# Optimization experiments

Hardware: AMD Instinct MI355X
Metric: run time of the kernel (lower is better)

## Reference

```python
import jax, jax.numpy as jnp
import numpy as np

EMA_BETA = 0.9
NUM_HEADS = 16

def causal_prefix_ema(x, beta):
    # x: [b, t, d]; s_t = beta*s_{t-1} + (1-beta)*x_t, s_{-1}=0
    def step(s, xt):
        s = beta * s + (1.0 - beta) * xt
        return s, s
    s0 = jnp.zeros_like(x[:, 0, :])
    _, ys = jax.lax.scan(step, s0, jnp.swapaxes(x, 0, 1))  # [t, b, d]
    return jnp.swapaxes(ys, 0, 1)

def setup_inputs() -> dict:
    key = jax.random.key(0)
    ks = jax.random.split(key, 9)
    b, t, d = 2, 1024, 2048
    sc = lambda fan_in: 1.0 / np.sqrt(fan_in)
    return {
        "x": jax.random.normal(ks[0], (b, t, d), jnp.float32),
        "l3_memory": jax.random.normal(ks[1], (b, 1, d), jnp.float32),
        "wq": jax.random.normal(ks[2], (d, d), jnp.float32) * sc(d),
        "wk": jax.random.normal(ks[3], (d, d), jnp.float32) * sc(d),
        "wv": jax.random.normal(ks[4], (d, d), jnp.float32) * sc(d),
        "wo": jax.random.normal(ks[5], (d, d), jnp.float32) * sc(d),
        "rw1": jax.random.normal(ks[6], (d // 2, d), jnp.float32) * sc(d),
        "rb1": jnp.zeros((d // 2,), jnp.float32),
        "rw2": jax.random.normal(ks[7], (3, d // 2), jnp.float32) * sc(d // 2),
        "rb2": jnp.zeros((3,), jnp.float32),
    }

def reference(x, l3_memory, wq, wk, wv, wo, rw1, rb1, rw2, rb2):
    b, t, d = x.shape
    h = NUM_HEADS
    dh = d // h
    scale = 1.0 / np.sqrt(dh)

    q = x @ wq.T                                   # [b,t,d]
    l1 = x
    l2 = causal_prefix_ema(x, EMA_BETA)            # [b,t,d]
    l3 = jnp.broadcast_to(l3_memory, (b, t, d))    # repeat retrieval memory to length t

    # router: MLP(Q) -> softmax over 3 levels
    hdn = jax.nn.silu(q @ rw1.T + rb1)
    lam = jax.nn.softmax(hdn @ rw2.T + rb2, axis=-1)  # [b,t,3]

    fused = lam[..., 0:1] * l1 + lam[..., 1:2] * l2 + lam[..., 2:3] * l3

    def heads(y):
        return jnp.swapaxes(y.reshape(b, t, h, dh), 1, 2)  # [b,h,t,dh]

    qh = heads(q)
    kh = heads(fused @ wk.T)
    vh = heads(fused @ wv.T)

    scores = jnp.einsum("bhqd,bhkd->bhqk", qh, kh) * scale
    causal = jnp.tril(jnp.ones((t, t), bool))
    scores = jnp.where(causal, scores, jnp.finfo(scores.dtype).min)
    attn = jax.nn.softmax(scores, axis=-1)
    out = jnp.einsum("bhqk,bhkd->bhqd", attn, vh)

    out = jnp.swapaxes(out, 1, 2).reshape(b, t, d) @ wo.T
    return (out, kh, vh, lam)
```

## Files before the change

### kernel.cpp

```cpp
#include <hip/hip_runtime.h>
#include <hip/hip_bf16.h>
#include <math.h>

#define B_  2
#define T_  1024
#define D_  2048
#define H_  16
#define DH_ 128
#define M_  2048
#define DR_ 1024
#define CH_  16
#define NCH_ 64

typedef __attribute__((ext_vector_type(8))) short short8;
typedef __attribute__((ext_vector_type(4))) short sh4;
typedef __attribute__((ext_vector_type(4))) float f32x4;

__device__ __forceinline__ void gld16(const __hip_bfloat16* g, __hip_bfloat16* l) {
  __builtin_amdgcn_global_load_lds(
      (const __attribute__((address_space(1))) unsigned int*)g,
      (__attribute__((address_space(3))) unsigned int*)l, 16, 0, 0);
}

template<int BM, int CMODE, bool SILU>
__global__ __launch_bounds__(256)
void gemm_mfma(const __hip_bfloat16* __restrict__ A,
               const __hip_bfloat16* __restrict__ Bm,
               const float* __restrict__ bias,
               float* __restrict__ C, __hip_bfloat16* __restrict__ Cb,
               float* __restrict__ C2, __hip_bfloat16* __restrict__ Cb2,
               int M, int N, int K)
{
  constexpr int NI = BM / 32;
  constexpr int AC = BM / 64;
  constexpr int ROWS = BM + 128;
  __shared__ __hip_bfloat16 AB[2][2][ROWS * 32];
  const int tid  = threadIdx.x;
  const int wave = tid >> 6;
  const int lane = tid & 63;
  const int m0 = blockIdx.y * BM;
  const int n0 = blockIdx.x * 128;
  const int wm = (wave >> 1) * (BM / 2);
  const int wn = (wave & 1) * 64;

  const int srow = lane >> 2;
  const int scol = (lane & 3) * 8;
  const __hip_bfloat16* Ag = A  + (size_t)(m0 + wave * (BM / 4) + srow) * K + scol;
  const __hip_bfloat16* Bg = Bm + (size_t)(n0 + wave * 32 + srow) * K + scol;

  const int fr = lane & 15;
  const int fk = (lane >> 4) * 8;

  f32x4 acc[NI][4];
  #pragma unroll
  for (int i = 0; i < NI; ++i)
    #pragma unroll
    for (int j = 0; j < 4; ++j) acc[i][j] = (f32x4)0.f;

  auto stage = [&](int bf, int k0) {
    #pragma unroll
    for (int h = 0; h < 2; ++h) {
      #pragma unroll
      for (int c = 0; c < AC; ++c)
        gld16(Ag + k0 + h * 32 + (size_t)(c * 16) * K,
              &AB[bf][h][(wave * (BM / 4) + c * 16) * 32]);
      #pragma unroll
      for (int c = 0; c < 2; ++c)
        gld16(Bg + k0 + h * 32 + (size_t)(c * 16) * K,
              &AB[bf][h][(BM + wave * 32 + c * 16) * 32]);
    }
  };

  stage(0, 0);
  __syncthreads();
  int cur = 0;
  for (int k0 = 0; k0 < K; k0 += 64) {
    if (k0 + 64 < K) stage(cur ^ 1, k0 + 64);
    #pragma unroll
    for (int h = 0; h < 2; ++h) {
      short8 af[NI], bfr[4];
      #pragma unroll
      for (int i = 0; i < NI; ++i)
        af[i]  = *(const short8*)&AB[cur][h][(wm + i * 16 + fr) * 32 + fk];
      #pragma unroll
      for (int j = 0; j < 4; ++j)
        bfr[j] = *(const short8*)&AB[cur][h][(BM + wn + j * 16 + fr) * 32 + fk];
      #pragma unroll
      for (int i = 0; i < NI; ++i)
        #pragma unroll
        for (int j = 0; j < 4; ++j)
          acc[i][j] = __builtin_amdgcn_mfma_f32_16x16x32_bf16(af[i], bfr[j], acc[i][j], 0, 0, 0);
    }
    __syncthreads();
    cur ^= 1;
  }

  if constexpr (CMODE == 4) {
    if (n0 >= D_) {
      __hip_bfloat16* flat = &AB[0][0][0];
      const int bb  = m0 >> 10, t0v = m0 & 1023;
      const int hh  = (n0 - D_) >> 7;
      #pragma unroll
      for (int i = 0; i < NI; ++i) {
        const int tl0 = wm + i * 16 + (lane >> 4) * 4;
        #pragma unroll
        for (int j = 0; j < 4; ++j) {
          const int ddl = wn + j * 16 + (lane & 15);
          __hip_bfloat16 tmp[4];
          #pragma unroll
          for (int r = 0; r < 4; ++r) {
            const float v = acc[i][j][r];
            C2[(((size_t)(bb * H_ + hh)) * T_ + t0v + tl0 + r) * DH_ + ddl] = v;
            tmp[r] = __float2bfloat16(v);
          }
          *(sh4*)(flat + ddl * 136 + tl0) = *(const sh4*)tmp;
        }
      }
      __syncthreads();
      const int dd = tid >> 1, th = (tid & 1) * 64;
      __hip_bfloat16* dst = Cb2 + (((size_t)(bb * H_ + hh)) * DH_ + dd) * T_ + t0v + th;
      const __hip_bfloat16* srcl = flat + dd * 136 + th;
      #pragma unroll
      for (int q = 0; q < 8; ++q)
        *(short8*)(dst + q * 8) = *(const short8*)(srcl + q * 8);
      return;
    }
  }

  #pragma unroll
  for (int i = 0; i < NI; ++i) {
    #pragma unroll
    for (int j = 0; j < 4; ++j) {
      const int row0 = m0 + wm + i * 16 + (lane >> 4) * 4;
      const int col  = n0 + wn + j * 16 + (lane & 15);
      float vr[4];
      #pragma unroll
      for (int r = 0; r < 4; ++r) {
        float v = acc[i][j][r];
        if (bias) v += bias[col];
        if (SILU) v = v / (1.f + __expf(-v));
        vr[r] = v;
      }
      if (CMODE == 0) {
        #pragma unroll
        for (int r = 0; r < 4; ++r) C[(size_t)(row0 + r) * N + col] = vr[r];
      } else if (CMODE == 1) {
        #pragma unroll
        for (int r = 0; r < 4; ++r) Cb[(size_t)(row0 + r) * N + col] = __float2bfloat16(vr[r]);
      } else {
        const int bb = row0 >> 10, t0v = row0 & 1023;
        const int hh = col >> 7, dd = col & 127;
        #pragma unroll
        for (int r = 0; r < 4; ++r) {
          const size_t idx = (((size_t)(bb * H_ + hh)) * T_ + t0v + r) * DH_ + dd;
          C[idx] = vr[r];
          Cb[idx] = __float2bfloat16(vr[r]);
        }
      }
    }
  }
}

__global__ __launch_bounds__(256)
void prep_all(const float* __restrict__ x, __hip_bfloat16* __restrict__ xb,
              float* __restrict__ l2, float* __restrict__ lf,
              const float* __restrict__ s1, const float* __restrict__ s2,
              const float* __restrict__ s3, const float* __restrict__ s4,
              const float* __restrict__ s5,
              __hip_bfloat16* d1, __hip_bfloat16* d2, __hip_bfloat16* d3,
              __hip_bfloat16* d4, __hip_bfloat16* d5,
              int n1, int n2, int n3, int n4, int n5)
{
  if (blockIdx.y == 0) {
    const int bid = blockIdx.x;
    if (bid >= 256) return;
    const int dblk = bid & 1;
    const int ch   = (bid >> 1) & 63;
    const int b    = bid >> 7;
    const int t0 = ch * CH_;
    const int d  = dblk * 1024 + threadIdx.x * 4;
    const float* xp = x  + (size_t)b * T_ * D_ + d;
    float*       lp = l2 + (size_t)b * T_ * D_ + d;
    __hip_bfloat16* xo = xb + (size_t)b * T_ * D_ + d;
    float4 s = make_float4(0.f, 0.f, 0.f, 0.f);
    #pragma unroll 4
    for (int t = t0; t < t0 + CH_; ++t) {
      float4 v = *(const float4*)(xp + (size_t)t * D_);
      __hip_bfloat16 tmp[4] = {__float2bfloat16(v.x), __float2bfloat16(v.y),
                               __float2bfloat16(v.z), __float2bfloat16(v.w)};
      *(sh4*)(xo + (size_t)t * D_) = *(const sh4*)tmp;
      s.x = 0.9f * s.x + 0.1f * v.x;
      s.y = 0.9f * s.y + 0.1f * v.y;
      s.z = 0.9f * s.z + 0.1f * v.z;
      s.w = 0.9f * s.w + 0.1f * v.w;
      *(float4*)(lp + (size_t)t * D_) = s;
    }
    *(float4*)(lf + ((size_t)b * NCH_ + ch) * D_ + d) = s;
    return;
  }
  const float* s; __hip_bfloat16* d; int n;
  switch (blockIdx.y) {
    case 1: s = s1; d = d1; n = n1; break;
    case 2: s = s2; d = d2; n = n2; break;
    case 3: s = s3; d = d3; n = n3; break;
    case 4: s = s4; d = d4; n = n4; break;
    default: s = s5; d = d5; n = n5; break;
  }
  const int i = (blockIdx.x * 256 + threadIdx.x) * 8;
  if (i < n) {
    float4 a = *(const float4*)(s + i);
    float4 b = *(const float4*)(s + i + 4);
    __hip_bfloat16 t[8] = {__float2bfloat16(a.x), __float2bfloat16(a.y),
                           __float2bfloat16(a.z), __float2bfloat16(a.w),
                           __float2bfloat16(b.x), __float2bfloat16(b.y),
                           __float2bfloat16(b.z), __float2bfloat16(b.w)};
    *(short8*)(d + i) = *(const short8*)t;
  }
}

__global__ __launch_bounds__(256)
void fuse_router(const float* __restrict__ x, const float* __restrict__ l2,
                 const float* __restrict__ l3m, const float* __restrict__ hdn,
                 const float* __restrict__ rw2, const float* __restrict__ rb2,
                 const float* __restrict__ lf, float* __restrict__ lam,
                 __hip_bfloat16* __restrict__ fb)
{
  __shared__ float lamS[8][3];
  const int tid = threadIdx.x;
  const int g = tid >> 5, l32 = tid & 31;
  const int m = blockIdx.x * 8 + g;
  const float* hp = hdn + (size_t)m * DR_;
  float s0 = 0.f, s1 = 0.f, s2 = 0.f;
  #pragma unroll
  for (int it = 0; it < 8; ++it) {
    const int k = l32 * 4 + it * 128;
    float4 h4 = *(const float4*)(hp + k);
    float4 w0 = *(const float4*)(rw2 + k);
    float4 w1 = *(const float4*)(rw2 + DR_ + k);
    float4 w2 = *(const float4*)(rw2 + 2 * DR_ + k);
    s0 += h4.x * w0.x + h4.y * w0.y + h4.z * w0.z + h4.w * w0.w;
    s1 += h4.x * w1.x + h4.y * w1.y + h4.z * w1.z + h4.w * w1.w;
    s2 += h4.x * w2.x + h4.y * w2.y + h4.z * w2.z + h4.w * w2.w;
  }
  #pragma unroll
  for (int off = 16; off > 0; off >>= 1) {
    s0 += __shfl_xor(s0, off);
    s1 += __shfl_xor(s1, off);
    s2 += __shfl_xor(s2, off);
  }
  if (l32 == 0) {
    s0 += rb2[0]; s1 += rb2[1]; s2 += rb2[2];
    float mx = fmaxf(s0, fmaxf(s1, s2));
    float e0 = __expf(s0 - mx), e1 = __expf(s1 - mx), e2 = __expf(s2 - mx);
    float inv = 1.f / (e0 + e1 + e2);
    lam[(size_t)m * 3 + 0] = e0 * inv;
    lam[(size_t)m * 3 + 1] = e1 * inv;
    lam[(size_t)m * 3 + 2] = e2 * inv;
    lamS[g][0] = e0 * inv; lamS[g][1] = e1 * inv; lamS[g][2] = e2 * inv;
  }

  const int m0b = blockIdx.x * 8;
  const int bb  = m0b >> 10;
  const int ch  = (m0b & 1023) >> 4;
  const int c   = tid * 8;
  float4 cv0 = make_float4(0.f, 0.f, 0.f, 0.f);
  float4 cv1 = make_float4(0.f, 0.f, 0.f, 0.f);
  {
    float w = 1.f;
    for (int j = ch - 1; j >= 0; --j) {
      const float* lp = lf + ((size_t)bb * NCH_ + j) * D_ + c;
      float4 a0 = *(const float4*)(lp);
      float4 a1 = *(const float4*)(lp + 4);
      cv0.x += w * a0.x; cv0.y += w * a0.y; cv0.z += w * a0.z; cv0.w += w * a0.w;
      cv1.x += w * a1.x; cv1.y += w * a1.y; cv1.z += w * a1.z; cv1.w += w * a1.w;
      w *= 0.18530201888518416f;
    }
  }
  __syncthreads();

  const int base = m0b & 15;
  #pragma unroll
  for (int r = 0; r < 8; ++r) {
    const int mm = m0b + r;
    const float pw = __expf((float)(base + r + 1) * -0.105360515657f);
    const float u0 = lamS[r][0], u1 = lamS[r][1], u2 = lamS[r][2];
    const float* xp = x   + (size_t)mm * D_ + c;
    const float* ep = l2  + (size_t)mm * D_ + c;
    const float* gp = l3m + (size_t)bb * D_ + c;
    __hip_bfloat16 tmp[8];
    {
      float4 xv = *(const float4*)(xp);
      float4 ev = *(const float4*)(ep);
      float4 gv = *(const float4*)(gp);
      tmp[0] = __float2bfloat16(u0 * xv.x + u1 * (ev.x + pw * cv0.x) + u2 * gv.x);
      tmp[1] = __float2bfloat16(u0 * xv.y + u1 * (ev.y + pw * cv0.y) + u2 * gv.y);
      tmp[2] = __float2bfloat16(u0 * xv.z + u1 * (ev.z + pw * cv0.z) + u2 * gv.z);
      tmp[3] = __float2bfloat16(u0 * xv.w + u1 * (ev.w + pw * cv0.w) + u2 * gv.w);
    }
    {
      float4 xv = *(const float4*)(xp + 4);
      float4 ev = *(const float4*)(ep + 4);
      float4 gv = *(const float4*)(gp + 4);
      tmp[4] = __float2bfloat16(u0 * xv.x + u1 * (ev.x + pw * cv1.x) + u2 * gv.x);
      tmp[5] = __float2bfloat16(u0 * xv.y + u1 * (ev.y + pw * cv1.y) + u2 * gv.y);
      tmp[6] = __float2bfloat16(u0 * xv.z + u1 * (ev.z + pw * cv1.z) + u2 * gv.z);
      tmp[7] = __float2bfloat16(u0 * xv.w + u1 * (ev.w + pw * cv1.w) + u2 * gv.w);
    }
    *(short8*)(fb + (size_t)mm * D_ + c) = *(const short8*)tmp;
  }
}

__global__ __launch_bounds__(256)
void flash_mfma(const __hip_bfloat16* __restrict__ qg,
                const __hip_bfloat16* __restrict__ kg,
                const __hip_bfloat16* __restrict__ vg,
                __hip_bfloat16* __restrict__ og)
{
  __shared__ __hip_bfloat16 Ks[2][64 * 136];
  __shared__ __hip_bfloat16 Vt[2][128 * 72];
  __shared__ __hip_bfloat16 Ps[64 * 72];
  const int tid  = threadIdx.x;
  const int wave = tid >> 6, lane = tid & 63;
  const int L    = blockIdx.x;
  const int halfg = L >> 8, idx = L & 255;
  const int bh = (idx >> 4) | (halfg << 4);
  const int qt = halfg ? (15 - (idx & 15)) : (idx & 15);
  const int b = bh >> 4, h = bh & 15;
  const int q0 = qt * 64;
  const int lo = lane & 15, hi = lane >> 4;

  short8 aq[4];
  {
    const __hip_bfloat16* qsrc = qg + (size_t)(b * T_ + q0 + wave * 16 + lo) * D_ + h * DH_;
    #pragma unroll
    for (int kk = 0; kk < 4; ++kk)
      aq[kk] = *(const short8*)(qsrc + kk * 32 + hi * 8);
  }

  f32x4 oacc[8];
  #pragma unroll
  for (int i = 0; i < 8; ++i) oacc[i] = (f32x4)0.f;
  float mrow[4]  = {-INFINITY, -INFINITY, -INFINITY, -INFINITY};
  float lrowp[4] = {0.f, 0.f, 0.f, 0.f};

  const __hip_bfloat16* kbp = kg + (size_t)bh * T_ * DH_;
  const __hip_bfloat16* vbp = vg + (size_t)bh * DH_ * T_;
  const float scale = 0.08838834764831845f;

  short8 kreg[4], vreg[4];
  auto load_tile = [&](int k0) {
    #pragma unroll
    for (int i = 0; i < 4; ++i) {
      const int ci = tid + 256 * i;
      const int r = ci >> 4, j = ci & 15;
      kreg[i] = *(const short8*)(kbp + (size_t)(k0 + r) * DH_ + j * 8);
      const int dd = ci >> 3, j2 = ci & 7;
      vreg[i] = *(const short8*)(vbp + (size_t)dd * T_ + k0 + j2 * 8);
    }
  };
  auto write_lds = [&](int bf) {
    #pragma unroll
    for (int i = 0; i < 4; ++i) {
      const int ci = tid + 256 * i;
      const int r = ci >> 4, j = ci & 15;
      *(short8*)&Ks[bf][r * 136 + j * 8] = kreg[i];
      const int dd = ci >> 3, j2 = ci & 7;
      *(short8*)&Vt[bf][dd * 72 + j2 * 8] = vreg[i];
    }
  };

  load_tile(0);
  write_lds(0);
  if (qt > 0) load_tile(64);
  __syncthreads();

  for (int kt = 0; kt <= qt; ++kt) {
    const int cur = kt & 1;
    f32x4 sc[4];
    __builtin_amdgcn_s_setprio(1);
    #pragma unroll
    for (int nt = 0; nt < 4; ++nt) {
      sc[nt] = (f32x4)0.f;
      #pragma unroll
      for (int kk = 0; kk < 4; ++kk) {
        short8 bk = *(const short8*)&Ks[cur][(nt * 16 + lo) * 136 + kk * 32 + hi * 8];
        sc[nt] = __builtin_amdgcn_mfma_f32_16x16x32_bf16(aq[kk], bk, sc[nt], 0, 0, 0);
      }
    }
    __builtin_amdgcn_s_setprio(0);
    #pragma unroll
    for (int nt = 0; nt < 4; ++nt)
      #pragma unroll
      for (int r = 0; r < 4; ++r) sc[nt][r] *= scale;
    if (kt == qt) {
      const int qrow = q0 + wave * 16 + hi * 4;
      #pragma unroll
      for (int nt = 0; nt < 4; ++nt) {
        const int key = qt * 64 + nt * 16 + lo;
        #pragma unroll
        for (int r = 0; r < 4; ++r)
          if (key > qrow + r) sc[nt][r] = -1e30f;
      }
    }
    float mxv[4];
    #pragma unroll
    for (int r = 0; r < 4; ++r) {
      float mx = fmaxf(fmaxf(sc[0][r], sc[1][r]), fmaxf(sc[2][r], sc[3][r]));
      mx = fmaxf(mx, __shfl_xor(mx, 1));
      mx = fmaxf(mx, __shfl_xor(mx, 2));
      mx = fmaxf(mx, __shfl_xor(mx, 4));
      mx = fmaxf(mx, __shfl_xor(mx, 8));
      mxv[r] = mx;
    }
    const bool deferLane = (mxv[0] <= mrow[0] + 8.f) & (mxv[1] <= mrow[1] + 8.f) &
                           (mxv[2] <= mrow[2] + 8.f) & (mxv[3] <= mrow[3] + 8.f);
    if (__all(deferLane)) {
      #pragma unroll
      for (int r = 0; r < 4; ++r) {
        float ls = 0.f;
        #pragma unroll
        for (int nt = 0; nt < 4; ++nt) {
          float p = __expf(sc[nt][r] - mrow[r]);
          sc[nt][r] = p;
          ls += p;
        }
        lrowp[r] += ls;
      }
    } else {
      float alpha[4];
      #pragma unroll
      for (int r = 0; r < 4; ++r) {
        const float nm = fmaxf(mrow[r], mxv[r]);
        alpha[r] = __expf(mrow[r] - nm);
        mrow[r] = nm;
        float ls = 0.f;
        #pragma unroll
        for (int nt = 0; nt < 4; ++nt) {
          float p = __expf(sc[nt][r] - nm);
          sc[nt][r] = p;
          ls += p;
        }
        lrowp[r] = lrowp[r] * alpha[r] + ls;
      }
      #pragma unroll
      for (int n2 = 0; n2 < 8; ++n2)
        #pragma unroll
        for (int r = 0; r < 4; ++r) oacc[n2][r] *= alpha[r];
    }
    #pragma unroll
    for (int nt = 0; nt < 4; ++nt)
      #pragma unroll
      for (int r = 0; r < 4; ++r)
        Ps[(wave * 16 + hi * 4 + r) * 72 + nt * 16 + lo] = __float2bfloat16(sc[nt][r]);
    short8 ap[2];
    #pragma unroll
    for (int k2 = 0; k2 < 2; ++k2)
      ap[k2] = *(const short8*)&Ps[(wave * 16 + lo) * 72 + k2 * 32 + hi * 8];
    __builtin_amdgcn_s_setprio(1);
    #pragma unroll
    for (int n2 = 0; n2 < 8; ++n2) {
      #pragma unroll
      for (int k2 = 0; k2 < 2; ++k2) {
        short8 bv = *(const short8*)&Vt[cur][(n2 * 16 + lo) * 72 + k2 * 32 + hi * 8];
        oacc[n2] = __builtin_amdgcn_mfma_f32_16x16x32_bf16(ap[k2], bv, oacc[n2], 0, 0, 0);
      }
    }
    __builtin_amdgcn_s_setprio(0);
    if (kt < qt) {
      write_lds(cur ^ 1);
      if (kt + 1 < qt) load_tile((kt + 2) * 64);
    }
    __syncthreads();
  }

  float inv[4];
  #pragma unroll
  for (int r = 0; r < 4; ++r) {
    float l = lrowp[r];
    l += __shfl_xor(l, 1);
    l += __shfl_xor(l, 2);
    l += __shfl_xor(l, 4);
    l += __shfl_xor(l, 8);
    inv[r] = 1.f / l;
  }
  __hip_bfloat16* od = og + (size_t)(b * T_ + q0 + wave * 16 + hi * 4) * D_ + h * DH_;
  #pragma unroll
  for (int n2 = 0; n2 < 8; ++n2)
    #pragma unroll
    for (int r = 0; r < 4; ++r)
      od[(size_t)r * D_ + n2 * 16 + lo] = __float2bfloat16(oacc[n2][r] * inv[r]);
}

extern "C" void kernel_launch(void* const* d_in, const int* in_sizes, int n_in,
                              void* d_out, int out_size, void* d_ws, size_t ws_size,
                              hipStream_t stream)
{
  const float* x   = (const float*)d_in[0];
  const float* l3m = (const float*)d_in[1];
  const float* wq  = (const float*)d_in[2];
  const float* wk  = (const float*)d_in[3];
  const float* wv  = (const float*)d_in[4];
  const float* wo  = (const float*)d_in[5];
  const float* rw1 = (const float*)d_in[6];
  const float* rb1 = (const float*)d_in[7];
  const float* rw2 = (const float*)d_in[8];
  const float* rb2 = (const float*)d_in[9];

  float* out = (float*)d_out;
  float* kh  = out + 4194304;
  float* vh  = out + 8388608;
  float* lam = out + 12582912;

  char* wsb = (char*)d_ws;
  float*          l2_f32 = (float*)(wsb);
  float*          hdn    = (float*)(wsb + (16u << 20));
  __hip_bfloat16* wkb    = (__hip_bfloat16*)(wsb + (24u << 20));
  __hip_bfloat16* wvb    = (__hip_bfloat16*)(wsb + (32u << 20));
  __hip_bfloat16* wob    = (__hip_bfloat16*)(wsb + (40u << 20));
  __hip_bfloat16* fusedb = (__hip_bfloat16*)(wsb + (48u << 20));
  __hip_bfloat16* attnb  = (__hip_bfloat16*)(wsb + (56u << 20));
  __hip_bfloat16* khb    = (__hip_bfloat16*)(wsb + (64u << 20));
  __hip_bfloat16* vtb    = (__hip_bfloat16*)(wsb + (72u << 20));
  float*          lf     = (float*)(wsb + (57u << 20));
  __hip_bfloat16* wqb  = (__hip_bfloat16*)kh;
  __hip_bfloat16* rw1b = (__hip_bfloat16*)kh + 4194304;
  __hip_bfloat16* xb   = (__hip_bfloat16*)vh;
  __hip_bfloat16* qb   = (__hip_bfloat16*)out;

  dim3 blk(256);

  prep_all<<<dim3(2048, 6), blk, 0, stream>>>(x, xb, l2_f32, lf,
                                              wq, wk, wv, wo, rw1,
                                              wqb, wkb, wvb, wob, rw1b,
                                              D_ * D_, D_ * D_, D_ * D_, D_ * D_, DR_ * D_);
  gemm_mfma<64, 1, false><<<dim3(16, 32), blk, 0, stream>>>(xb, wqb, nullptr, nullptr, qb, nullptr, nullptr, M_, D_, D_);
  gemm_mfma<64, 0, true><<<dim3(8, 32), blk, 0, stream>>>(qb, rw1b, rb1, hdn, nullptr, nullptr, nullptr, M_, DR_, D_);
  fuse_router<<<dim3(256), blk, 0, stream>>>(x, l2_f32, l3m, hdn, rw2, rb2, lf, lam, fusedb);
  gemm_mfma<128, 4, false><<<dim3(32, 16), blk, 0, stream>>>(fusedb, wkb, nullptr, kh, khb, vh, vtb, M_, 2 * D_, D_);
  flash_mfma<<<dim3(512), blk, 0, stream>>>(qb, khb, vtb, attnb);
  gemm_mfma<64, 0, false><<<dim3(16, 32), blk, 0, stream>>>(attnb, wob, nullptr, out, nullptr, nullptr, nullptr, M_, D_, D_);
}
```

Measured before the change: 321.0 us.

## Recompute EMA in fuse_router and overlap weight conversion with router GEMM

Stops writing the full fp32 EMA tensor (l2) in prep_all. fuse_router instead rebuilds the within-chunk EMA by rescanning up to 15 prior rows of x, which removes a 16 MB write and a 16 MB read. The wk/wv/wo fp32-to-bf16 conversions move out of prep_all into extra blocks (blockIdx.z==1) of the router-hidden GEMM launch, so they run alongside that GEMM and not before the q GEMM. The cost is redundant x reads in fuse_router and GEMM launches that mix two kinds of work.

```diff
diff --git a/kernel.cpp b/kernel.cpp
--- a/kernel.cpp
+++ b/kernel.cpp
@@ -22,15 +22,41 @@
       (__attribute__((address_space(3))) unsigned int*)l, 16, 0, 0);
 }
 
-template<int BM, int CMODE, bool SILU>
+template<int BM, int CMODE, bool SILU, bool CVTW>
 __global__ __launch_bounds__(256)
 void gemm_mfma(const __hip_bfloat16* __restrict__ A,
                const __hip_bfloat16* __restrict__ Bm,
                const float* __restrict__ bias,
                float* __restrict__ C, __hip_bfloat16* __restrict__ Cb,
                float* __restrict__ C2, __hip_bfloat16* __restrict__ Cb2,
+               const float* __restrict__ cw0, const float* __restrict__ cw1,
+               const float* __restrict__ cw2,
+               __hip_bfloat16* __restrict__ dw0, __hip_bfloat16* __restrict__ dw1,
+               __hip_bfloat16* __restrict__ dw2,
                int M, int N, int K)
 {
+  if constexpr (CVTW) {
+    if (blockIdx.z == 1) {
+      const int bid = blockIdx.y * gridDim.x + blockIdx.x;
+      const float* s_[3] = {cw0, cw1, cw2};
+      __hip_bfloat16* d_[3] = {dw0, dw1, dw2};
+      #pragma unroll
+      for (int w = 0; w < 3; ++w) {
+        for (int chunk = bid; chunk < 2048; chunk += 256) {
+          const int i = chunk * 2048 + threadIdx.x * 8;
+          float4 a = *(const float4*)(s_[w] + i);
+          float4 b = *(const float4*)(s_[w] + i + 4);
+          __hip_bfloat16 t[8] = {__float2bfloat16(a.x), __float2bfloat16(a.y),
+                                 __float2bfloat16(a.z), __float2bfloat16(a.w),
+                                 __float2bfloat16(b.x), __float2bfloat16(b.y),
+                                 __float2bfloat16(b.z), __float2bfloat16(b.w)};
+          *(short8*)(d_[w] + i) = *(const short8*)t;
+        }
+      }
+      return;
+    }
+  }
+
   constexpr int NI = BM / 32;
   constexpr int AC = BM / 64;
   constexpr int ROWS = BM + 128;
@@ -163,13 +189,10 @@
 
 __global__ __launch_bounds__(256)
 void prep_all(const float* __restrict__ x, __hip_bfloat16* __restrict__ xb,
-              float* __restrict__ l2, float* __restrict__ lf,
+              float* __restrict__ lf,
               const float* __restrict__ s1, const float* __restrict__ s2,
-              const float* __restrict__ s3, const float* __restrict__ s4,
-              const float* __restrict__ s5,
-              __hip_bfloat16* d1, __hip_bfloat16* d2, __hip_bfloat16* d3,
-              __hip_bfloat16* d4, __hip_bfloat16* d5,
-              int n1, int n2, int n3, int n4, int n5)
+              __hip_bfloat16* d1, __hip_bfloat16* d2,
+              int n1, int n2)
 {
   if (blockIdx.y == 0) {
     const int bid = blockIdx.x;
@@ -180,7 +203,6 @@
     const int t0 = ch * CH_;
     const int d  = dblk * 1024 + threadIdx.x * 4;
     const float* xp = x  + (size_t)b * T_ * D_ + d;
-    float*       lp = l2 + (size_t)b * T_ * D_ + d;
     __hip_bfloat16* xo = xb + (size_t)b * T_ * D_ + d;
     float4 s = make_float4(0.f, 0.f, 0.f, 0.f);
     #pragma unroll 4
@@ -193,19 +215,13 @@
       s.y = 0.9f * s.y + 0.1f * v.y;
       s.z = 0.9f * s.z + 0.1f * v.z;
       s.w = 0.9f * s.w + 0.1f * v.w;
-      *(float4*)(lp + (size_t)t * D_) = s;
     }
     *(float4*)(lf + ((size_t)b * NCH_ + ch) * D_ + d) = s;
     return;
   }
   const float* s; __hip_bfloat16* d; int n;
-  switch (blockIdx.y) {
-    case 1: s = s1; d = d1; n = n1; break;
-    case 2: s = s2; d = d2; n = n2; break;
-    case 3: s = s3; d = d3; n = n3; break;
-    case 4: s = s4; d = d4; n = n4; break;
-    default: s = s5; d = d5; n = n5; break;
-  }
+  if (blockIdx.y == 1) { s = s1; d = d1; n = n1; }
+  else                 { s = s2; d = d2; n = n2; }
   const int i = (blockIdx.x * 256 + threadIdx.x) * 8;
   if (i < n) {
     float4 a = *(const float4*)(s + i);
@@ -219,7 +235,7 @@
 }
 
 __global__ __launch_bounds__(256)
-void fuse_router(const float* __restrict__ x, const float* __restrict__ l2,
+void fuse_router(const float* __restrict__ x,
                  const float* __restrict__ l3m, const float* __restrict__ hdn,
                  const float* __restrict__ rw2, const float* __restrict__ rb2,
                  const float* __restrict__ lf, float* __restrict__ lam,
@@ -262,6 +278,7 @@
   const int m0b = blockIdx.x * 8;
   const int bb  = m0b >> 10;
   const int ch  = (m0b & 1023) >> 4;
+  const int base = m0b & 15;
   const int c   = tid * 8;
   float4 cv0 = make_float4(0.f, 0.f, 0.f, 0.f);
   float4 cv1 = make_float4(0.f, 0.f, 0.f, 0.f);
@@ -278,33 +295,45 @@
   }
   __syncthreads();
 
-  const int base = m0b & 15;
+  float4 e0v = make_float4(0.f, 0.f, 0.f, 0.f);
+  float4 e1v = make_float4(0.f, 0.f, 0.f, 0.f);
+  const float* xbase = x + (size_t)(m0b - base) * D_ + c;
+  for (int j = 0; j < base; ++j) {
+    float4 a0 = *(const float4*)(xbase + (size_t)j * D_);
+    float4 a1 = *(const float4*)(xbase + (size_t)j * D_ + 4);
+    e0v.x = 0.9f * e0v.x + 0.1f * a0.x; e0v.y = 0.9f * e0v.y + 0.1f * a0.y;
+    e0v.z = 0.9f * e0v.z + 0.1f * a0.z; e0v.w = 0.9f * e0v.w + 0.1f * a0.w;
+    e1v.x = 0.9f * e1v.x + 0.1f * a1.x; e1v.y = 0.9f * e1v.y + 0.1f * a1.y;
+    e1v.z = 0.9f * e1v.z + 0.1f * a1.z; e1v.w = 0.9f * e1v.w + 0.1f * a1.w;
+  }
+
+  const float* gp = l3m + (size_t)bb * D_ + c;
+  const float4 gv0 = *(const float4*)(gp);
+  const float4 gv1 = *(const float4*)(gp + 4);
   #pragma unroll
   for (int r = 0; r < 8; ++r) {
     const int mm = m0b + r;
     const float pw = __expf((float)(base + r + 1) * -0.105360515657f);
     const float u0 = lamS[r][0], u1 = lamS[r][1], u2 = lamS[r][2];
-    const float* xp = x   + (size_t)mm * D_ + c;
-    const float* ep = l2  + (size_t)mm * D_ + c;
-    const float* gp = l3m + (size_t)bb * D_ + c;
+    const float* xp = x + (size_t)mm * D_ + c;
     __hip_bfloat16 tmp[8];
     {
       float4 xv = *(const float4*)(xp);
-      float4 ev = *(const float4*)(ep);
-      float4 gv = *(const float4*)(gp);
-      tmp[0] = __float2bfloat16(u0 * xv.x + u1 * (ev.x + pw * cv0.x) + u2 * gv.x);
-      tmp[1] = __float2bfloat16(u0 * xv.y + u1 * (ev.y + pw * cv0.y) + u2 * gv.y);
-      tmp[2] = __float2bfloat16(u0 * xv.z + u1 * (ev.z + pw * cv0.z) + u2 * gv.z);
-      tmp[3] = __float2bfloat16(u0 * xv.w + u1 * (ev.w + pw * cv0.w) + u2 * gv.w);
+      e0v.x = 0.9f * e0v.x + 0.1f * xv.x; e0v.y = 0.9f * e0v.y + 0.1f * xv.y;
+      e0v.z = 0.9f * e0v.z + 0.1f * xv.z; e0v.w = 0.9f * e0v.w + 0.1f * xv.w;
+      tmp[0] = __float2bfloat16(u0 * xv.x + u1 * (e0v.x + pw * cv0.x) + u2 * gv0.x);
+      tmp[1] = __float2bfloat16(u0 * xv.y + u1 * (e0v.y + pw * cv0.y) + u2 * gv0.y);
+      tmp[2] = __float2bfloat16(u0 * xv.z + u1 * (e0v.z + pw * cv0.z) + u2 * gv0.z);
+      tmp[3] = __float2bfloat16(u0 * xv.w + u1 * (e0v.w + pw * cv0.w) + u2 * gv0.w);
     }
     {
       float4 xv = *(const float4*)(xp + 4);
-      float4 ev = *(const float4*)(ep + 4);
-      float4 gv = *(const float4*)(gp + 4);
-      tmp[4] = __float2bfloat16(u0 * xv.x + u1 * (ev.x + pw * cv1.x) + u2 * gv.x);
-      tmp[5] = __float2bfloat16(u0 * xv.y + u1 * (ev.y + pw * cv1.y) + u2 * gv.y);
-      tmp[6] = __float2bfloat16(u0 * xv.z + u1 * (ev.z + pw * cv1.z) + u2 * gv.z);
-      tmp[7] = __float2bfloat16(u0 * xv.w + u1 * (ev.w + pw * cv1.w) + u2 * gv.w);
+      e1v.x = 0.9f * e1v.x + 0.1f * xv.x; e1v.y = 0.9f * e1v.y + 0.1f * xv.y;
+      e1v.z = 0.9f * e1v.z + 0.1f * xv.z; e1v.w = 0.9f * e1v.w + 0.1f * xv.w;
+      tmp[4] = __float2bfloat16(u0 * xv.x + u1 * (e1v.x + pw * cv1.x) + u2 * gv1.x);
+      tmp[5] = __float2bfloat16(u0 * xv.y + u1 * (e1v.y + pw * cv1.y) + u2 * gv1.y);
+      tmp[6] = __float2bfloat16(u0 * xv.z + u1 * (e1v.z + pw * cv1.z) + u2 * gv1.z);
+      tmp[7] = __float2bfloat16(u0 * xv.w + u1 * (e1v.w + pw * cv1.w) + u2 * gv1.w);
     }
     *(short8*)(fb + (size_t)mm * D_ + c) = *(const short8*)tmp;
   }
@@ -512,7 +541,6 @@
   float* lam = out + 12582912;
 
   char* wsb = (char*)d_ws;
-  float*          l2_f32 = (float*)(wsb);
   float*          hdn    = (float*)(wsb + (16u << 20));
   __hip_bfloat16* wkb    = (__hip_bfloat16*)(wsb + (24u << 20));
   __hip_bfloat16* wvb    = (__hip_bfloat16*)(wsb + (32u << 20));
@@ -521,7 +549,7 @@
   __hip_bfloat16* attnb  = (__hip_bfloat16*)(wsb + (56u << 20));
   __hip_bfloat16* khb    = (__hip_bfloat16*)(wsb + (64u << 20));
   __hip_bfloat16* vtb    = (__hip_bfloat16*)(wsb + (72u << 20));
-  float*          lf     = (float*)(wsb + (57u << 20));
+  float*          lf     = (float*)(wsb);
   __hip_bfloat16* wqb  = (__hip_bfloat16*)kh;
   __hip_bfloat16* rw1b = (__hip_bfloat16*)kh + 4194304;
   __hip_bfloat16* xb   = (__hip_bfloat16*)vh;
@@ -529,14 +557,20 @@
 
   dim3 blk(256);
 
-  prep_all<<<dim3(2048, 6), blk, 0, stream>>>(x, xb, l2_f32, lf,
-                                              wq, wk, wv, wo, rw1,
-                                              wqb, wkb, wvb, wob, rw1b,
-                                              D_ * D_, D_ * D_, D_ * D_, D_ * D_, DR_ * D_);
-  gemm_mfma<64, 1, false><<<dim3(16, 32), blk, 0, stream>>>(xb, wqb, nullptr, nullptr, qb, nullptr, nullptr, M_, D_, D_);
-  gemm_mfma<64, 0, true><<<dim3(8, 32), blk, 0, stream>>>(qb, rw1b, rb1, hdn, nullptr, nullptr, nullptr, M_, DR_, D_);
-  fuse_router<<<dim3(256), blk, 0, stream>>>(x, l2_f32, l3m, hdn, rw2, rb2, lf, lam, fusedb);
-  gemm_mfma<128, 4, false><<<dim3(32, 16), blk, 0, stream>>>(fusedb, wkb, nullptr, kh, khb, vh, vtb, M_, 2 * D_, D_);
+  prep_all<<<dim3(2048, 3), blk, 0, stream>>>(x, xb, lf, wq, rw1, wqb, rw1b,
+                                              D_ * D_, DR_ * D_);
+  gemm_mfma<64, 1, false, false><<<dim3(16, 32), blk, 0, stream>>>(
+      xb, wqb, nullptr, nullptr, qb, nullptr, nullptr,
+      nullptr, nullptr, nullptr, nullptr, nullptr, nullptr, M_, D_, D_);
+  gemm_mfma<64, 0, true, true><<<dim3(8, 32, 2), blk, 0, stream>>>(
+      qb, rw1b, rb1, hdn, nullptr, nullptr, nullptr,
+      wk, wv, wo, wkb, wvb, wob, M_, DR_, D_);
+  fuse_router<<<dim3(256), blk, 0, stream>>>(x, l3m, hdn, rw2, rb2, lf, lam, fusedb);
+  gemm_mfma<128, 4, false, false><<<dim3(32, 16), blk, 0, stream>>>(
+      fusedb, wkb, nullptr, kh, khb, vh, vtb,
+      nullptr, nullptr, nullptr, nullptr, nullptr, nullptr, M_, 2 * D_, D_);
   flash_mfma<<<dim3(512), blk, 0, stream>>>(qb, khb, vtb, attnb);
-  gemm_mfma<64, 0, false><<<dim3(16, 32), blk, 0, stream>>>(attnb, wob, nullptr, out, nullptr, nullptr, nullptr, M_, D_, D_);
+  gemm_mfma<64, 0, false, false><<<dim3(16, 32), blk, 0, stream>>>(
+      attnb, wob, nullptr, out, nullptr, nullptr, nullptr,
+      nullptr, nullptr, nullptr, nullptr, nullptr, nullptr, M_, D_, D_);
 }
```

Result: faster. 308.2 us (-4.0%).
